# Performance work log

Measured on AMD Instinct MI355X. Metric: run time of the kernel, lower is better.

The kernel has to match this reference:

```python
import jax, jax.numpy as jnp
import numpy as np

TAU_U = 1.0
TAU_L = 0.05
EPS = 1e-12  # torch F.normalize eps


def setup_inputs() -> dict:
    key = jax.random.key(0)
    ks = jax.random.split(key, 8)
    N, D, B = 100000, 128, 8192
    x1 = jax.random.normal(ks[0], (N, D), dtype=jnp.float32)
    x2 = jax.random.normal(ks[1], (N, D), dtype=jnp.float32)
    x1_index = jax.random.randint(ks[2], (B,), 0, N, dtype=jnp.int64 if jax.config.jax_enable_x64 else jnp.int32)
    x2_index = jax.random.randint(ks[3], (B,), 0, N, dtype=jnp.int64 if jax.config.jax_enable_x64 else jnp.int32)
    # Linear params (torch Linear default init: U(-1/sqrt(fan_in), 1/sqrt(fan_in)))
    lim1 = 1.0 / np.sqrt(D)
    W1 = jax.random.uniform(ks[4], (D, D), minval=-lim1, maxval=lim1, dtype=jnp.float32)
    b1 = jax.random.uniform(ks[5], (D,), minval=-lim1, maxval=lim1, dtype=jnp.float32)
    W2 = jax.random.uniform(ks[6], (1, D), minval=-lim1, maxval=lim1, dtype=jnp.float32)
    b2 = jax.random.uniform(ks[7], (1,), minval=-lim1, maxval=lim1, dtype=jnp.float32)
    return {"x1": x1, "x2": x2, "x1_index": x1_index, "x2_index": x2_index,
            "W1": W1, "b1": b1, "W2": W2, "b2": b2}


def _l2norm(x):
    # matches torch F.normalize(dim=1) for 2-D input
    n = jnp.sqrt(jnp.sum(x * x, axis=-1, keepdims=True))
    return x / jnp.maximum(n, EPS)


def reference(x1, x2, x1_index, x2_index, W1, b1, W2, b2):
    x1_feat = _l2norm(x1[x1_index])          # [B, D]
    x2_feat = _l2norm(x2[x2_index])          # [B, D]

    h = x1_feat * x2_feat                    # [B, D]
    h = h @ W1.T + b1                        # lin1
    h = jnp.where(h >= 0, h, 0.2 * h)        # leaky_relu(0.2)
    s = jax.nn.sigmoid(h @ W2.T + b2)        # [B, 1]
    ssl_temp = (TAU_U - TAU_L) * (1.0 - s) + TAU_L   # [B, 1]

    pos = jnp.sum(x1_feat * x2_feat, axis=-1)         # [B]
    # NOTE: [B] / [B,1] broadcasts to [B,B] exactly like torch
    pos_rating = jnp.exp(pos / ssl_temp)              # [B, B]

    tot = x1_feat @ x2_feat.T                          # [B, B]
    tot_rating = jnp.sum(jnp.exp(tot / ssl_temp), axis=1)  # [B]

    ssl_temp_avg = jnp.mean(ssl_temp)
    return (pos_rating, tot_rating, ssl_temp_avg)
```

## Files before the change

### kernel.cpp

```cpp
#include <hip/hip_runtime.h>
#include <stdint.h>

typedef __bf16 bf16x8 __attribute__((ext_vector_type(8)));
typedef float f32x4 __attribute__((ext_vector_type(4)));
typedef __attribute__((address_space(3))) uint32_t as3u32;
typedef const __attribute__((address_space(1))) uint32_t as1u32;

#define B_TOT 8192
#define DD 128
#define OUT_TOT 67108864UL
#define OUT_AVG 67117056UL

__device__ inline unsigned short f2bf(float x){
  union { float f; uint32_t u; } v; v.f = x;
  return (unsigned short)((v.u + 0x7fffu + ((v.u >> 16) & 1u)) >> 16);
}

__device__ inline float bsum128(float v, volatile float* s2){
  #pragma unroll
  for (int o = 32; o; o >>= 1) v += __shfl_xor(v, o);
  __syncthreads();
  if ((threadIdx.x & 63) == 0) s2[threadIdx.x >> 6] = v;
  __syncthreads();
  return s2[0] + s2[1];
}

__global__ __launch_bounds__(128) void k_feat(const float* __restrict__ x1,
    const float* __restrict__ x2, const int* __restrict__ i1a, const int* __restrict__ i2a,
    unsigned short* __restrict__ f1b, unsigned short* __restrict__ f2b,
    unsigned short* __restrict__ hb, float* __restrict__ posw, float* __restrict__ out){
  __shared__ float s2[2];
  int b = blockIdx.x, t = threadIdx.x;
  int gid = b * 128 + t;
  if (gid <= 8192) out[OUT_TOT + gid] = 0.f;
  size_t r1 = (size_t)i1a[b] * DD, r2 = (size_t)i2a[b] * DD;
  float v1 = x1[r1 + t], v2 = x2[r2 + t];
  float n1 = sqrtf(bsum128(v1 * v1, s2));
  float f1 = v1 / fmaxf(n1, 1e-12f);
  float n2 = sqrtf(bsum128(v2 * v2, s2));
  float f2 = v2 / fmaxf(n2, 1e-12f);
  float h = f1 * f2;
  float pos = bsum128(h, s2);
  int o = b * DD + t;
  f1b[o] = f2bf(f1); f2b[o] = f2bf(f2); hb[o] = f2bf(h);
  if (t == 0) posw[b] = pos;
}

__device__ inline void stage_tile(const unsigned short* g, unsigned short* s){
  int tid = threadIdx.x;
  #pragma unroll
  for (int it = 0; it < 8; ++it){
    int c = tid + it * 256;
    int row = c >> 4, cc = c & 15;
    int src = (row << 4) + (cc ^ (row & 7));
    __builtin_amdgcn_global_load_lds((as1u32*)(g + src * 8),
                                     (as3u32*)(s + c * 8), 16, 0, 0);
  }
}

__device__ inline void mfma_tile(const unsigned short* As, const unsigned short* Bs,
                                 f32x4 acc[4][4]){
  int tid = threadIdx.x;
  int w = tid >> 6, l = tid & 63;
  int wr = (w >> 1) * 64, wc = (w & 1) * 64;
  int lo = l & 15, hi = l >> 4;
  f32x4 zero = {0.f, 0.f, 0.f, 0.f};
  #pragma unroll
  for (int m = 0; m < 4; ++m)
    #pragma unroll
    for (int n = 0; n < 4; ++n) acc[m][n] = zero;
  #pragma unroll
  for (int kk = 0; kk < 4; ++kk){
    bf16x8 af[4], bfv[4];
    #pragma unroll
    for (int m = 0; m < 4; ++m){
      int row = wr + m * 16 + lo;
      af[m] = *(const bf16x8*)(As + row * 128 + ((kk * 4 + hi) ^ (row & 7)) * 8);
    }
    #pragma unroll
    for (int n = 0; n < 4; ++n){
      int row = wc + n * 16 + lo;
      bfv[n] = *(const bf16x8*)(Bs + row * 128 + ((kk * 4 + hi) ^ (row & 7)) * 8);
    }
    #pragma unroll
    for (int m = 0; m < 4; ++m)
      #pragma unroll
      for (int n = 0; n < 4; ++n)
        acc[m][n] = __builtin_amdgcn_mfma_f32_16x16x32_bf16(af[m], bfv[n], acc[m][n], 0, 0, 0);
  }
}

__global__ __launch_bounds__(256) void k_lin(const unsigned short* __restrict__ hb,
    const float* __restrict__ W1, const float* __restrict__ b1,
    const float* __restrict__ W2, const float* __restrict__ b2,
    float* __restrict__ rTw, float* __restrict__ out){
  __shared__ __align__(16) unsigned short As[16384];
  __shared__ __align__(16) unsigned short Bs[16384];
  __shared__ float zpart[2][128];
  __shared__ float s4[4];
  int i0 = blockIdx.x * 128;
  int tid = threadIdx.x;
  stage_tile(hb + (size_t)i0 * 128, As);
  #pragma unroll
  for (int it = 0; it < 8; ++it){
    int c = tid + it * 256;
    int row = c >> 4, cc = c & 15;
    int src = (row << 4) + (cc ^ (row & 7));
    const float4* g4 = (const float4*)(W1 + src * 8);
    float4 a = g4[0], b = g4[1];
    unsigned short t8[8];
    t8[0] = f2bf(a.x); t8[1] = f2bf(a.y); t8[2] = f2bf(a.z); t8[3] = f2bf(a.w);
    t8[4] = f2bf(b.x); t8[5] = f2bf(b.y); t8[6] = f2bf(b.z); t8[7] = f2bf(b.w);
    *(uint4*)(Bs + c * 8) = *(uint4*)t8;
  }
  asm volatile("s_waitcnt vmcnt(0)" ::: "memory");
  __syncthreads();
  f32x4 acc[4][4];
  mfma_tile(As, Bs, acc);
  int w = tid >> 6, l = tid & 63;
  int wrb = (w >> 1) * 64, wcb = (w & 1) * 64, lo = l & 15, hi = l >> 4;
  float w2v[4], b1v[4];
  #pragma unroll
  for (int n = 0; n < 4; ++n){ int col = wcb + n * 16 + lo; w2v[n] = W2[col]; b1v[n] = b1[col]; }
  #pragma unroll
  for (int m = 0; m < 4; ++m){
    #pragma unroll
    for (int q = 0; q < 4; ++q){
      float p = 0.f;
      #pragma unroll
      for (int n = 0; n < 4; ++n){
        float hv = acc[m][n][q] + b1v[n];
        hv = hv >= 0.f ? hv : 0.2f * hv;
        p += hv * w2v[n];
      }
      p += __shfl_xor(p, 1); p += __shfl_xor(p, 2);
      p += __shfl_xor(p, 4); p += __shfl_xor(p, 8);
      if (lo == 0) zpart[w & 1][wrb + m * 16 + hi * 4 + q] = p;
    }
  }
  __syncthreads();
  float Tloc = 0.f;
  if (tid < 128){
    float z = zpart[0][tid] + zpart[1][tid] + b2[0];
    float s = 1.f / (1.f + __expf(-z));
    float T = 0.95f * (1.f - s) + 0.05f;
    rTw[i0 + tid] = 1.f / T;
    Tloc = T;
  }
  float v = Tloc;
  #pragma unroll
  for (int o = 32; o; o >>= 1) v += __shfl_xor(v, o);
  if ((tid & 63) == 0) s4[tid >> 6] = v;
  __syncthreads();
  if (tid == 0) atomicAdd(out + OUT_AVG, (s4[0] + s4[1] + s4[2] + s4[3]) * (1.0f / 8192.0f));
}

__global__ __launch_bounds__(256, 4) void k_tot(const unsigned short* __restrict__ f1b,
    const unsigned short* __restrict__ f2b, const float* __restrict__ rTw,
    const float* __restrict__ posw, float* __restrict__ out){
  __shared__ __align__(16) unsigned short Bs[16384];
  __shared__ float rowacc[2][128];
  __shared__ float posS[128];
  __shared__ float rS[128];
  int bx = (blockIdx.x & 7) * 512 + (blockIdx.x >> 3);
  int rt = bx >> 6, ct = bx & 63;
  int tid = threadIdx.x, w = tid >> 6, l = tid & 63;
  int wr = (w >> 1) * 64, wc = (w & 1) * 64;
  int lo = l & 15, hi = l >> 4;
  stage_tile(f2b + (size_t)ct * 16384, Bs);
  if (tid < 128) posS[tid] = posw[ct * 128 + tid];
  else           rS[tid - 128] = rTw[rt * 128 + tid - 128];
  const unsigned short* Ag = f1b + (size_t)rt * 16384;
  f32x4 acc[4][4];
  f32x4 zero = {0.f, 0.f, 0.f, 0.f};
  #pragma unroll
  for (int m = 0; m < 4; ++m)
    #pragma unroll
    for (int n = 0; n < 4; ++n) acc[m][n] = zero;
  asm volatile("s_waitcnt vmcnt(0)" ::: "memory");
  __syncthreads();
  #pragma unroll
  for (int kk = 0; kk < 4; ++kk){
    bf16x8 af[4], bfv[4];
    #pragma unroll
    for (int m = 0; m < 4; ++m){
      int row = wr + m * 16 + lo;
      af[m] = *(const bf16x8*)(Ag + row * 128 + (kk * 4 + hi) * 8);
    }
    #pragma unroll
    for (int n = 0; n < 4; ++n){
      int row = wc + n * 16 + lo;
      bfv[n] = *(const bf16x8*)(Bs + row * 128 + ((kk * 4 + hi) ^ (row & 7)) * 8);
    }
    #pragma unroll
    for (int m = 0; m < 4; ++m)
      #pragma unroll
      for (int n = 0; n < 4; ++n)
        acc[m][n] = __builtin_amdgcn_mfma_f32_16x16x32_bf16(af[m], bfv[n], acc[m][n], 0, 0, 0);
  }
  int wrb = wr;
  #pragma unroll
  for (int m = 0; m < 4; ++m){
    #pragma unroll
    for (int q = 0; q < 4; ++q){
      int lr = wrb + m * 16 + hi * 4 + q;
      float r = rS[lr];
      float p = __expf(acc[m][0][q] * r) + __expf(acc[m][1][q] * r)
              + __expf(acc[m][2][q] * r) + __expf(acc[m][3][q] * r);
      p += __shfl_xor(p, 1); p += __shfl_xor(p, 2);
      p += __shfl_xor(p, 4); p += __shfl_xor(p, 8);
      if (lo == 0) rowacc[w & 1][lr] = p;
    }
  }
  __syncthreads();
  if (tid < 128) atomicAdd(out + OUT_TOT + rt * 128 + tid, rowacc[0][tid] + rowacc[1][tid]);
  int c0 = (tid & 31) * 4;
  f32x4 p4 = *(const f32x4*)&posS[c0];
  #pragma unroll
  for (int pass = 0; pass < 16; ++pass){
    int row = pass * 8 + (tid >> 5);
    float r = rS[row];
    f32x4 e;
    e.x = __expf(p4.x * r); e.y = __expf(p4.y * r);
    e.z = __expf(p4.z * r); e.w = __expf(p4.w * r);
    __builtin_nontemporal_store(e, (f32x4*)(out + (size_t)(rt * 128 + row) * B_TOT + ct * 128 + c0));
  }
}

extern "C" void kernel_launch(void* const* d_in, const int* in_sizes, int n_in,
                              void* d_out, int out_size, void* d_ws, size_t ws_size,
                              hipStream_t stream){
  const float* x1 = (const float*)d_in[0];
  const float* x2 = (const float*)d_in[1];
  const int*   i1 = (const int*)d_in[2];
  const int*   i2 = (const int*)d_in[3];
  const float* W1 = (const float*)d_in[4];
  const float* b1 = (const float*)d_in[5];
  const float* W2 = (const float*)d_in[6];
  const float* b2 = (const float*)d_in[7];
  float* out = (float*)d_out;
  char* ws = (char*)d_ws;
  unsigned short* hb   = (unsigned short*)(ws);
  unsigned short* f1b  = (unsigned short*)(ws + 2097152);
  unsigned short* f2b  = (unsigned short*)(ws + 4194304);
  float* posw  = (float*)(ws + 6291456);
  float* rTw   = (float*)(ws + 6324224);

  hipLaunchKernelGGL(k_feat,  dim3(8192), dim3(128), 0, stream, x1, x2, i1, i2, f1b, f2b, hb, posw, out);
  hipLaunchKernelGGL(k_lin,   dim3(64),   dim3(256), 0, stream, hb, W1, b1, W2, b2, rTw, out);
  hipLaunchKernelGGL(k_tot,   dim3(4096), dim3(256), 0, stream, f1b, f2b, rTw, posw, out);
}
```

Baseline: 95.36 us.

## Make k_tot persistent over 8 column tiles with register-resident A fragments

Each block now handles one row tile and loops over 8 column tiles instead of one tile pair. The A fragments are loaded once from LDS into registers, and each B tile is staged into a single shared buffer. The staging load for the next tile is issued before the exp and store work on the current tile, so the load overlaps with that work. Row sums accumulate in registers and are flushed with fewer atomics. This cuts the grid from 4096 to 512 blocks and lowers occupancy to 2 blocks per SIMD bound. That risks less latency hiding, especially since the next tile's load is waited on at the top of each iteration.

```diff
diff --git a/kernel.cpp b/kernel.cpp
--- a/kernel.cpp
+++ b/kernel.cpp
@@ -155,76 +155,90 @@
   if (tid == 0) atomicAdd(out + OUT_AVG, (s4[0] + s4[1] + s4[2] + s4[3]) * (1.0f / 8192.0f));
 }
 
-__global__ __launch_bounds__(256, 4) void k_tot(const unsigned short* __restrict__ f1b,
+__global__ __launch_bounds__(256, 2) void k_tot(const unsigned short* __restrict__ f1b,
     const unsigned short* __restrict__ f2b, const float* __restrict__ rTw,
     const float* __restrict__ posw, float* __restrict__ out){
-  __shared__ __align__(16) unsigned short Bs[16384];
-  __shared__ float rowacc[2][128];
-  __shared__ float posS[128];
+  __shared__ __align__(16) unsigned short Buf[16384];
   __shared__ float rS[128];
-  int bx = (blockIdx.x & 7) * 512 + (blockIdx.x >> 3);
-  int rt = bx >> 6, ct = bx & 63;
+  int s = (blockIdx.x & 7) * 64 + (blockIdx.x >> 3);
+  int rt = s & 63, ctg = s >> 6;
   int tid = threadIdx.x, w = tid >> 6, l = tid & 63;
   int wr = (w >> 1) * 64, wc = (w & 1) * 64;
   int lo = l & 15, hi = l >> 4;
-  stage_tile(f2b + (size_t)ct * 16384, Bs);
-  if (tid < 128) posS[tid] = posw[ct * 128 + tid];
-  else           rS[tid - 128] = rTw[rt * 128 + tid - 128];
-  const unsigned short* Ag = f1b + (size_t)rt * 16384;
-  f32x4 acc[4][4];
-  f32x4 zero = {0.f, 0.f, 0.f, 0.f};
-  #pragma unroll
-  for (int m = 0; m < 4; ++m)
-    #pragma unroll
-    for (int n = 0; n < 4; ++n) acc[m][n] = zero;
+  stage_tile(f1b + (size_t)rt * 16384, Buf);
+  if (tid < 128) rS[tid] = rTw[rt * 128 + tid];
   asm volatile("s_waitcnt vmcnt(0)" ::: "memory");
   __syncthreads();
-  #pragma unroll
-  for (int kk = 0; kk < 4; ++kk){
-    bf16x8 af[4], bfv[4];
+  bf16x8 af[4][4];
+  #pragma unroll
+  for (int kk = 0; kk < 4; ++kk)
     #pragma unroll
     for (int m = 0; m < 4; ++m){
       int row = wr + m * 16 + lo;
-      af[m] = *(const bf16x8*)(Ag + row * 128 + (kk * 4 + hi) * 8);
-    }
-    #pragma unroll
-    for (int n = 0; n < 4; ++n){
-      int row = wc + n * 16 + lo;
-      bfv[n] = *(const bf16x8*)(Bs + row * 128 + ((kk * 4 + hi) ^ (row & 7)) * 8);
-    }
+      af[kk][m] = *(const bf16x8*)(Buf + row * 128 + ((kk * 4 + hi) ^ (row & 7)) * 8);
+    }
+  asm volatile("s_waitcnt lgkmcnt(0)" ::: "memory");
+  __syncthreads();
+  stage_tile(f2b + (size_t)(ctg * 8) * 16384, Buf);
+  float pacc[4][4] = {{0.f,0.f,0.f,0.f},{0.f,0.f,0.f,0.f},{0.f,0.f,0.f,0.f},{0.f,0.f,0.f,0.f}};
+  int prow = tid >> 5, pcol = (tid & 31) * 4;
+  #pragma unroll 1
+  for (int c8 = 0; c8 < 8; ++c8){
+    int ct = ctg * 8 + c8;
+    f32x4 p4 = *(const f32x4*)(posw + ct * 128 + pcol);
+    asm volatile("s_waitcnt vmcnt(0)" ::: "memory");
+    __syncthreads();
+    f32x4 acc[4][4];
+    f32x4 zero = {0.f,0.f,0.f,0.f};
     #pragma unroll
     for (int m = 0; m < 4; ++m)
       #pragma unroll
-      for (int n = 0; n < 4; ++n)
-        acc[m][n] = __builtin_amdgcn_mfma_f32_16x16x32_bf16(af[m], bfv[n], acc[m][n], 0, 0, 0);
-  }
-  int wrb = wr;
-  #pragma unroll
-  for (int m = 0; m < 4; ++m){
+      for (int n = 0; n < 4; ++n) acc[m][n] = zero;
+    #pragma unroll
+    for (int kk = 0; kk < 4; ++kk){
+      bf16x8 bfv[4];
+      #pragma unroll
+      for (int n = 0; n < 4; ++n){
+        int row = wc + n * 16 + lo;
+        bfv[n] = *(const bf16x8*)(Buf + row * 128 + ((kk * 4 + hi) ^ (row & 7)) * 8);
+      }
+      #pragma unroll
+      for (int m = 0; m < 4; ++m)
+        #pragma unroll
+        for (int n = 0; n < 4; ++n)
+          acc[m][n] = __builtin_amdgcn_mfma_f32_16x16x32_bf16(af[kk][m], bfv[n], acc[m][n], 0, 0, 0);
+    }
+    asm volatile("s_waitcnt lgkmcnt(0)" ::: "memory");
+    __syncthreads();
+    if (c8 < 7) stage_tile(f2b + (size_t)(ct + 1) * 16384, Buf);
+    #pragma unroll
+    for (int m = 0; m < 4; ++m)
+      #pragma unroll
+      for (int q = 0; q < 4; ++q){
+        float r = rS[wr + m * 16 + hi * 4 + q];
+        pacc[m][q] += __expf(acc[m][0][q] * r) + __expf(acc[m][1][q] * r)
+                    + __expf(acc[m][2][q] * r) + __expf(acc[m][3][q] * r);
+      }
+    float* obase = out + (size_t)(rt * 128) * B_TOT + ct * 128 + pcol;
+    #pragma unroll
+    for (int pass = 0; pass < 16; ++pass){
+      int row = pass * 8 + prow;
+      float r = rS[row];
+      f32x4 e;
+      e.x = __expf(p4.x * r); e.y = __expf(p4.y * r);
+      e.z = __expf(p4.z * r); e.w = __expf(p4.w * r);
+      __builtin_nontemporal_store(e, (f32x4*)(obase + (size_t)row * B_TOT));
+    }
+  }
+  #pragma unroll
+  for (int m = 0; m < 4; ++m)
     #pragma unroll
     for (int q = 0; q < 4; ++q){
-      int lr = wrb + m * 16 + hi * 4 + q;
-      float r = rS[lr];
-      float p = __expf(acc[m][0][q] * r) + __expf(acc[m][1][q] * r)
-              + __expf(acc[m][2][q] * r) + __expf(acc[m][3][q] * r);
+      float p = pacc[m][q];
       p += __shfl_xor(p, 1); p += __shfl_xor(p, 2);
       p += __shfl_xor(p, 4); p += __shfl_xor(p, 8);
-      if (lo == 0) rowacc[w & 1][lr] = p;
-    }
-  }
-  __syncthreads();
-  if (tid < 128) atomicAdd(out + OUT_TOT + rt * 128 + tid, rowacc[0][tid] + rowacc[1][tid]);
-  int c0 = (tid & 31) * 4;
-  f32x4 p4 = *(const f32x4*)&posS[c0];
-  #pragma unroll
-  for (int pass = 0; pass < 16; ++pass){
-    int row = pass * 8 + (tid >> 5);
-    float r = rS[row];
-    f32x4 e;
-    e.x = __expf(p4.x * r); e.y = __expf(p4.y * r);
-    e.z = __expf(p4.z * r); e.w = __expf(p4.w * r);
-    __builtin_nontemporal_store(e, (f32x4*)(out + (size_t)(rt * 128 + row) * B_TOT + ct * 128 + c0));
-  }
+      if (lo == 0) atomicAdd(out + OUT_TOT + rt * 128 + wr + m * 16 + hi * 4 + q, p);
+    }
 }
 
 extern "C" void kernel_launch(void* const* d_in, const int* in_sizes, int n_in,
@@ -248,5 +262,5 @@
 
   hipLaunchKernelGGL(k_feat,  dim3(8192), dim3(128), 0, stream, x1, x2, i1, i2, f1b, f2b, hb, posw, out);
   hipLaunchKernelGGL(k_lin,   dim3(64),   dim3(256), 0, stream, hb, W1, b1, W2, b2, rTw, out);
-  hipLaunchKernelGGL(k_tot,   dim3(4096), dim3(256), 0, stream, f1b, f2b, rTw, posw, out);
-}
+  hipLaunchKernelGGL(k_tot,   dim3(512),  dim3(256), 0, stream, f1b, f2b, rTw, posw, out);
+}
```

New measurement: 91.10 us. 4.5% less time.
